# Performance work log

Hardware: AMD Instinct MI355X
Metric: run time of the kernel (lower is better)

The kernel has to match this reference:

```python
import jax, jax.numpy as jnp
import numpy as np

N_NODES = 50000
N_EDGES = 800000
IN_DIM = 128
EMB = 64
EDGE_DIM = 6
N_LAYERS = 4
OUT_DIM = 1


def setup_inputs() -> dict:
    key = jax.random.key(0)
    ks = jax.random.split(key, 20)
    s = 0.05
    inp = {
        "x": jax.random.normal(ks[0], (N_NODES, IN_DIM), jnp.float32),
        "edge_index": jax.random.randint(ks[1], (2, N_EDGES), 0, N_NODES, jnp.int64),
        "edge_attr": jax.random.normal(ks[2], (N_EDGES, EDGE_DIM), jnp.float32),
        # input projection
        "lin_in_w": jax.random.normal(ks[3], (IN_DIM, EMB), jnp.float32) * s,
        "lin_in_b": jnp.zeros((EMB,), jnp.float32),
        # stacked per-layer MLP params: message MLP psi: (2*EMB+EDGE_DIM)->EMB->EMB
        "msg_w1": jax.random.normal(ks[4], (N_LAYERS, 2 * EMB + EDGE_DIM, EMB), jnp.float32) * s,
        "msg_b1": jnp.zeros((N_LAYERS, EMB), jnp.float32),
        "msg_w2": jax.random.normal(ks[5], (N_LAYERS, EMB, EMB), jnp.float32) * s,
        "msg_b2": jnp.zeros((N_LAYERS, EMB), jnp.float32),
        # update MLP phi: (2*EMB)->EMB->EMB
        "upd_w1": jax.random.normal(ks[6], (N_LAYERS, 2 * EMB, EMB), jnp.float32) * s,
        "upd_b1": jnp.zeros((N_LAYERS, EMB), jnp.float32),
        "upd_w2": jax.random.normal(ks[7], (N_LAYERS, EMB, EMB), jnp.float32) * s,
        "upd_b2": jnp.zeros((N_LAYERS, EMB), jnp.float32),
        # output head
        "pred_w": jax.random.normal(ks[8], (EMB, OUT_DIM), jnp.float32) * s,
        "pred_b": jnp.zeros((OUT_DIM,), jnp.float32),
    }
    return inp


def reference(x, edge_index, edge_attr, lin_in_w, lin_in_b,
              msg_w1, msg_b1, msg_w2, msg_b2,
              upd_w1, upd_b1, upd_w2, upd_b2,
              pred_w, pred_b):
    n = x.shape[0]
    src = edge_index[0]  # h_j: source nodes
    dst = edge_index[1]  # h_i: target nodes (aggregation index in PyG default flow)
    h = x @ lin_in_w + lin_in_b  # (n, EMB)
    n_layers = msg_w1.shape[0]
    for l in range(n_layers):
        # message: psi([h_i, h_j, e_ij])  -> (E, EMB)
        m = jnp.concatenate([h[dst], h[src], edge_attr], axis=-1)
        m = jax.nn.relu(m @ msg_w1[l] + msg_b1[l])
        m = jax.nn.relu(m @ msg_w2[l] + msg_b2[l])
        # aggregate: scatter-add over target nodes
        agg = jax.ops.segment_sum(m, dst, num_segments=n)
        # update: phi([h, m_i]) with residual connection (h = h + conv(h))
        u = jnp.concatenate([h, agg], axis=-1)
        u = jax.nn.relu(u @ upd_w1[l] + upd_b1[l])
        u = jax.nn.relu(u @ upd_w2[l] + upd_b2[l])
        h = h + u
    out = h @ pred_w + pred_b  # (n, OUT_DIM)
    return jnp.sum(out, axis=-2)  # (OUT_DIM,)
```

## Files before the change

kernel.cpp:

```cpp
#include <hip/hip_runtime.h>


typedef __attribute__((ext_vector_type(8))) short short8;
typedef __attribute__((ext_vector_type(4))) float float4v;

__device__ __forceinline__ unsigned short f2bf(float f) {
    unsigned int u = __float_as_uint(f);
    unsigned int r = u + 0x7fff + ((u >> 16) & 1);
    return (unsigned short)(r >> 16);
}
__device__ __forceinline__ float bf2f(unsigned short u) {
    return __uint_as_float(((unsigned int)u) << 16);
}

#define MFMA16(a, b, c) __builtin_amdgcn_mfma_f32_16x16x32_bf16(a, b, c, 0, 0, 0)

struct bfpair { short hi, lo; };
__device__ __forceinline__ bfpair wsplit(float wv) {
    bfpair p;
    unsigned short h = f2bf(wv);
    float hf = __uint_as_float(((unsigned int)h) << 16);
    p.hi = (short)h;
    p.lo = (short)f2bf(wv - hf);
    return p;
}

#define WP_TOTAL 106496
#define OFF_IN   0
#define OFF_PRE(l)  (8192  + (l) * 8192)
#define OFF_MW2(l)  (40960 + (l) * 4096)
#define OFF_UW1(l)  (57344 + (l) * 8192)
#define OFF_UW2(l)  (90112 + (l) * 4096)

__global__ __launch_bounds__(256) void k_wprep(const float* __restrict__ lin_w,
        const float* __restrict__ mw1, const float* __restrict__ mw2,
        const float* __restrict__ uw1, const float* __restrict__ uw2,
        unsigned short* __restrict__ H, unsigned short* __restrict__ L) {
    const int tid = blockIdx.x * 256 + threadIdx.x;
    if (tid >= WP_TOTAL) return;
    float val;
    if (tid < 8192) {
        int rem = tid;
        int nt = rem >> 11, kf = (rem >> 9) & 3;
        int lane = (rem >> 3) & 63, j = rem & 7;
        int k = kf * 32 + (lane >> 4) * 8 + j;
        val = lin_w[k * 64 + nt * 16 + (lane & 15)];
    } else if (tid < 40960) {
        int t = tid - 8192, layer = t >> 13, rem = t & 8191;
        int nt = rem >> 10, kf = (rem >> 9) & 1;
        int lane = (rem >> 3) & 63, j = rem & 7;
        int k = kf * 32 + (lane >> 4) * 8 + j;
        const float* w1 = mw1 + (size_t)layer * 134 * 64;
        val = (nt < 4) ? w1[k * 64 + nt * 16 + (lane & 15)]
                       : w1[(64 + k) * 64 + (nt - 4) * 16 + (lane & 15)];
    } else if (tid < 57344) {
        int t = tid - 40960, layer = t >> 12, rem = t & 4095;
        int nt = rem >> 10, kf = (rem >> 9) & 1;
        int lane = (rem >> 3) & 63, j = rem & 7;
        int k = kf * 32 + (lane >> 4) * 8 + j;
        val = mw2[(size_t)layer * 4096 + k * 64 + nt * 16 + (lane & 15)];
    } else if (tid < 90112) {
        int t = tid - 57344, layer = t >> 13, rem = t & 8191;
        int nt = rem >> 11, kf = (rem >> 9) & 3;
        int lane = (rem >> 3) & 63, j = rem & 7;
        int k = kf * 32 + (lane >> 4) * 8 + j;
        val = uw1[(size_t)layer * 8192 + k * 64 + nt * 16 + (lane & 15)];
    } else {
        int t = tid - 90112, layer = t >> 12, rem = t & 4095;
        int nt = rem >> 10, kf = (rem >> 9) & 1;
        int lane = (rem >> 3) & 63, j = rem & 7;
        int k = kf * 32 + (lane >> 4) * 8 + j;
        val = uw2[(size_t)layer * 4096 + k * 64 + nt * 16 + (lane & 15)];
    }
    bfpair p = wsplit(val);
    H[tid] = (unsigned short)p.hi;
    L[tid] = (unsigned short)p.lo;
}

#define LOADFRAG(dst, arr, nt, KF, kf) \
    dst = *(const short8*)&arr[((((nt) * (KF)) + (kf)) * 64 + lane) * 8]

__global__ __launch_bounds__(256) void k_hist(const int* __restrict__ dst,
        int* __restrict__ deg, int nEdges) {
    int e = blockIdx.x * blockDim.x + threadIdx.x;
    if (e < nEdges) atomicAdd(&deg[dst[e]], 1);
}

__global__ __launch_bounds__(256) void k_scan1(const int* __restrict__ deg,
        int* __restrict__ local, int* __restrict__ bsum, int nNodes) {
    __shared__ int sm[256];
    const int t = threadIdx.x;
    const int n = blockIdx.x * 256 + t;
    int v = (n < nNodes) ? deg[n] : 0;
    sm[t] = v;
    __syncthreads();
    for (int off = 1; off < 256; off <<= 1) {
        int u = (t >= off) ? sm[t - off] : 0;
        __syncthreads();
        sm[t] += u;
        __syncthreads();
    }
    if (n < nNodes) local[n] = sm[t] - v;
    if (t == 255) bsum[blockIdx.x] = sm[255];
}

__global__ __launch_bounds__(256) void k_scan2(int* __restrict__ bsum, int nB) {
    __shared__ int sm[256];
    const int t = threadIdx.x;
    int v = (t < nB) ? bsum[t] : 0;
    sm[t] = v;
    __syncthreads();
    for (int off = 1; off < 256; off <<= 1) {
        int u = (t >= off) ? sm[t - off] : 0;
        __syncthreads();
        sm[t] += u;
        __syncthreads();
    }
    if (t < nB) bsum[t] = sm[t] - v;
}

__global__ __launch_bounds__(256) void k_scan3(const int* __restrict__ local,
        const int* __restrict__ bsum, int* __restrict__ cursor, int nNodes) {
    int n = blockIdx.x * 256 + threadIdx.x;
    if (n < nNodes) cursor[n] = bsum[blockIdx.x] + local[n];
}

__global__ __launch_bounds__(256) void k_scatter(const int* __restrict__ src,
        const int* __restrict__ dst, const float* __restrict__ ea,
        int* __restrict__ cursor, int* __restrict__ col_src,
        int* __restrict__ dst_s, float* __restrict__ ea_s, int nEdges) {
    int e = blockIdx.x * blockDim.x + threadIdx.x;
    if (e < nEdges) {
        int d = dst[e];
        int pos = atomicAdd(&cursor[d], 1);
        col_src[pos] = src[e];
        dst_s[pos] = d;
        const float* p = ea + (size_t)e * 6;
        float* q = ea_s + (size_t)pos * 6;
#pragma unroll
        for (int j = 0; j < 6; ++j) q[j] = p[j];
    }
}


__global__ __launch_bounds__(256) void k_in(const float* __restrict__ x,
        const unsigned short* __restrict__ wh, const unsigned short* __restrict__ wl,
        const float* __restrict__ bia, float* __restrict__ h, int nNodes) {
    const int lane = threadIdx.x & 63;
    const int wib  = threadIdx.x >> 6;
    const int quad = lane >> 4, col = lane & 15;
    __shared__ unsigned short sm[4][16 * 136];
    unsigned short* __restrict__ mt = sm[wib];

    short8 bh[4][4], bl[4][4];
#pragma unroll
    for (int nt = 0; nt < 4; ++nt)
#pragma unroll
        for (int kf = 0; kf < 4; ++kf) {
            LOADFRAG(bh[nt][kf], wh, nt, 4, kf);
            LOADFRAG(bl[nt][kf], wl, nt, 4, kf);
        }
    float bv[4];
#pragma unroll
    for (int nt = 0; nt < 4; ++nt) bv[nt] = bia[nt * 16 + col];

    const int nTiles = (nNodes + 15) >> 4;
    const int wid = blockIdx.x * 4 + wib;
    const int nw  = gridDim.x * 4;
    for (int tile = wid; tile < nTiles; tile += nw) {
        const int base = tile * 16;
#pragma unroll
        for (int j = 0; j < 16; ++j) {
            int row = min(base + j, nNodes - 1);
            mt[j * 136 + lane]      = f2bf(x[(size_t)row * 128 + lane]);
            mt[j * 136 + 64 + lane] = f2bf(x[(size_t)row * 128 + 64 + lane]);
        }
        __builtin_amdgcn_s_waitcnt(0);
        short8 a[4];
#pragma unroll
        for (int kf = 0; kf < 4; ++kf)
            a[kf] = *(const short8*)&mt[col * 136 + kf * 32 + quad * 8];
#pragma unroll
        for (int nt = 0; nt < 4; ++nt) {
            float4v c = {0.f, 0.f, 0.f, 0.f};
#pragma unroll
            for (int kf = 0; kf < 4; ++kf) c = MFMA16(a[kf], bh[nt][kf], c);
#pragma unroll
            for (int kf = 0; kf < 4; ++kf) c = MFMA16(a[kf], bl[nt][kf], c);
#pragma unroll
            for (int r = 0; r < 4; ++r) {
                int row = base + quad * 4 + r;
                if (row < nNodes)
                    h[(size_t)row * 64 + nt * 16 + col] = c[r] + bv[nt];
            }
        }
    }
}

__global__ __launch_bounds__(256) void k_pre(const float* __restrict__ h,
        const unsigned short* __restrict__ wh, const unsigned short* __restrict__ wl,
        const float* __restrict__ b1m,
        unsigned short* __restrict__ P, unsigned short* __restrict__ Q,
        int nNodes) {
    const int lane = threadIdx.x & 63;
    const int wib  = threadIdx.x >> 6;
    const int quad = lane >> 4, col = lane & 15;
    __shared__ unsigned short sm[4][16 * 72];
    unsigned short* __restrict__ mt = sm[wib];

    short8 bh[8][2], bl[8][2];
#pragma unroll
    for (int nt = 0; nt < 8; ++nt)
#pragma unroll
        for (int kf = 0; kf < 2; ++kf) {
            LOADFRAG(bh[nt][kf], wh, nt, 2, kf);
            LOADFRAG(bl[nt][kf], wl, nt, 2, kf);
        }
    float bv1[4];
#pragma unroll
    for (int nt = 0; nt < 4; ++nt) bv1[nt] = b1m[nt * 16 + col];

    const int nTiles = (nNodes + 15) >> 4;
    const int wid = blockIdx.x * 4 + wib;
    const int nw  = gridDim.x * 4;
    for (int tile = wid; tile < nTiles; tile += nw) {
        const int base = tile * 16;
#pragma unroll
        for (int j = 0; j < 16; ++j) {
            int row = min(base + j, nNodes - 1);
            mt[j * 72 + lane] = f2bf(h[(size_t)row * 64 + lane]);
        }
        __builtin_amdgcn_s_waitcnt(0);
        short8 a0 = *(const short8*)&mt[col * 72 + quad * 8];
        short8 a1 = *(const short8*)&mt[col * 72 + 32 + quad * 8];
#pragma unroll
        for (int nt = 0; nt < 8; ++nt) {
            float4v c = {0.f, 0.f, 0.f, 0.f};
            c = MFMA16(a0, bh[nt][0], c);
            c = MFMA16(a1, bh[nt][1], c);
            c = MFMA16(a0, bl[nt][0], c);
            c = MFMA16(a1, bl[nt][1], c);
            unsigned short* __restrict__ outp = (nt < 4) ? P : Q;
            const int nc = (nt & 3) * 16 + col;
            const float badd = (nt < 4) ? bv1[nt & 3] : 0.f;
#pragma unroll
            for (int r = 0; r < 4; ++r) {
                int row = base + quad * 4 + r;
                if (row < nNodes) outp[(size_t)row * 64 + nc] = f2bf(c[r] + badd);
            }
        }
    }
}

__global__ __launch_bounds__(256) void k_upd1(const float* __restrict__ h,
        const float* __restrict__ agg,
        const unsigned short* __restrict__ wh, const unsigned short* __restrict__ wl,
        const float* __restrict__ b1, float* __restrict__ tv, int nNodes) {
    const int lane = threadIdx.x & 63;
    const int wib  = threadIdx.x >> 6;
    const int quad = lane >> 4, col = lane & 15;
    __shared__ unsigned short sm[4][16 * 136];
    unsigned short* __restrict__ mt = sm[wib];

    short8 bh[4][4], bl[4][4];
#pragma unroll
    for (int nt = 0; nt < 4; ++nt)
#pragma unroll
        for (int kf = 0; kf < 4; ++kf) {
            LOADFRAG(bh[nt][kf], wh, nt, 4, kf);
            LOADFRAG(bl[nt][kf], wl, nt, 4, kf);
        }
    float bv[4];
#pragma unroll
    for (int nt = 0; nt < 4; ++nt) bv[nt] = b1[nt * 16 + col];

    const int nTiles = (nNodes + 15) >> 4;
    const int wid = blockIdx.x * 4 + wib;
    const int nw  = gridDim.x * 4;
    for (int tile = wid; tile < nTiles; tile += nw) {
        const int base = tile * 16;
#pragma unroll
        for (int j = 0; j < 16; ++j) {
            int row = min(base + j, nNodes - 1);
            mt[j * 136 + lane]      = f2bf(h[(size_t)row * 64 + lane]);
            mt[j * 136 + 64 + lane] = f2bf(agg[(size_t)row * 64 + lane]);
        }
        __builtin_amdgcn_s_waitcnt(0);
        short8 a[4];
#pragma unroll
        for (int kf = 0; kf < 4; ++kf)
            a[kf] = *(const short8*)&mt[col * 136 + kf * 32 + quad * 8];
#pragma unroll
        for (int nt = 0; nt < 4; ++nt) {
            float4v c = {0.f, 0.f, 0.f, 0.f};
#pragma unroll
            for (int kf = 0; kf < 4; ++kf) c = MFMA16(a[kf], bh[nt][kf], c);
#pragma unroll
            for (int kf = 0; kf < 4; ++kf) c = MFMA16(a[kf], bl[nt][kf], c);
#pragma unroll
            for (int r = 0; r < 4; ++r) {
                int row = base + quad * 4 + r;
                if (row < nNodes)
                    tv[(size_t)row * 64 + nt * 16 + col] = fmaxf(c[r] + bv[nt], 0.f);
            }
        }
    }
}

__global__ __launch_bounds__(256) void k_upd2(float* __restrict__ h,
        float* __restrict__ tv,
        const unsigned short* __restrict__ wh, const unsigned short* __restrict__ wl,
        const float* __restrict__ b2, float* __restrict__ colsum,
        int nNodes, int doCS) {
    const int lane = threadIdx.x & 63;
    const int wib  = threadIdx.x >> 6;
    const int quad = lane >> 4, col = lane & 15;
    __shared__ unsigned short sm[4][16 * 72];
    unsigned short* __restrict__ mt = sm[wib];

    short8 bh[4][2], bl[4][2];
#pragma unroll
    for (int nt = 0; nt < 4; ++nt)
#pragma unroll
        for (int kf = 0; kf < 2; ++kf) {
            LOADFRAG(bh[nt][kf], wh, nt, 2, kf);
            LOADFRAG(bl[nt][kf], wl, nt, 2, kf);
        }
    float bv[4];
#pragma unroll
    for (int nt = 0; nt < 4; ++nt) bv[nt] = b2[nt * 16 + col];

    float cs0 = 0.f, cs1 = 0.f, cs2 = 0.f, cs3 = 0.f;
    const int nTiles = (nNodes + 15) >> 4;
    const int wid = blockIdx.x * 4 + wib;
    const int nw  = gridDim.x * 4;
    for (int tile = wid; tile < nTiles; tile += nw) {
        const int base = tile * 16;
#pragma unroll
        for (int j = 0; j < 16; ++j) {
            int row = min(base + j, nNodes - 1);
            mt[j * 72 + lane] = f2bf(tv[(size_t)row * 64 + lane]);
        }
        __builtin_amdgcn_s_waitcnt(0);
#pragma unroll
        for (int j = 0; j < 16; ++j) {
            int row = base + j;
            if (row < nNodes) tv[(size_t)row * 64 + lane] = 0.f;
        }
        short8 a0 = *(const short8*)&mt[col * 72 + quad * 8];
        short8 a1 = *(const short8*)&mt[col * 72 + 32 + quad * 8];
#pragma unroll
        for (int nt = 0; nt < 4; ++nt) {
            float4v c = {0.f, 0.f, 0.f, 0.f};
            c = MFMA16(a0, bh[nt][0], c);
            c = MFMA16(a1, bh[nt][1], c);
            c = MFMA16(a0, bl[nt][0], c);
            c = MFMA16(a1, bl[nt][1], c);
#pragma unroll
            for (int r = 0; r < 4; ++r) {
                int row = base + quad * 4 + r;
                if (row < nNodes) {
                    float* hp = &h[(size_t)row * 64 + nt * 16 + col];
                    float hn = *hp + fmaxf(c[r] + bv[nt], 0.f);
                    *hp = hn;
                    cs0 += (nt == 0) ? hn : 0.f;
                    cs1 += (nt == 1) ? hn : 0.f;
                    cs2 += (nt == 2) ? hn : 0.f;
                    cs3 += (nt == 3) ? hn : 0.f;
                }
            }
        }
    }
    if (doCS) {
        cs0 += __shfl_xor(cs0, 16); cs0 += __shfl_xor(cs0, 32);
        cs1 += __shfl_xor(cs1, 16); cs1 += __shfl_xor(cs1, 32);
        cs2 += __shfl_xor(cs2, 16); cs2 += __shfl_xor(cs2, 32);
        cs3 += __shfl_xor(cs3, 16); cs3 += __shfl_xor(cs3, 32);
        const float tot = (quad == 0) ? cs0 : (quad == 1) ? cs1
                        : (quad == 2) ? cs2 : cs3;
        atomicAdd(&colsum[lane], tot);
    }
}

#define EST 72

__global__ __launch_bounds__(512, 6) void k_edge(const unsigned short* __restrict__ P,
        const unsigned short* __restrict__ Q, const float* __restrict__ ea_s,
        const int* __restrict__ col_src, const int* __restrict__ dst_s,
        const float* __restrict__ w1e,
        const unsigned short* __restrict__ wh, const unsigned short* __restrict__ wl,
        const float* __restrict__ b2,
        float* __restrict__ agg, int nEdges) {
    const int lane = threadIdx.x & 63;
    const int wib  = threadIdx.x >> 6;
    const int wid  = blockIdx.x * 8 + wib;
    const int nw   = gridDim.x * 8;
    const int quad = lane >> 4;
    const int col  = lane & 15;
    const int li   = lane & 31;

    __shared__ unsigned short m1b[8][32 * EST];
    __shared__ unsigned short wB[8192];
    unsigned short* __restrict__ mt = m1b[wib];

    {
        const short8* __restrict__ sH = (const short8*)wh;
        const short8* __restrict__ sL = (const short8*)wl;
        short8* __restrict__ dB = (short8*)wB;
        dB[threadIdx.x]       = sH[threadIdx.x];
        dB[512 + threadIdx.x] = sL[threadIdx.x];
    }
    __syncthreads();

    float w1ec[6];
#pragma unroll
    for (int j = 0; j < 6; ++j) w1ec[j] = w1e[j * 64 + lane];

    float b2v[4];
#pragma unroll
    for (int nt = 0; nt < 4; ++nt) b2v[nt] = b2[nt * 16 + col];

    const int nBatch = (nEdges + 31) >> 5;
    const int per = nBatch / nw, rem = nBatch % nw;
    const int btLo = wid * per + min(wid, rem);
    const int btHi = btLo + per + (wid < rem ? 1 : 0);

    for (int bt = btLo; bt < btHi; ++bt) {
        const int base = __builtin_amdgcn_readfirstlane(bt << 5);
        const int gidx = min(base + li, nEdges - 1);
        const int vdj = dst_s[gidx];
        const int vsj = col_src[gidx];
        const int vprev = __shfl_up(vdj, 1);
        unsigned long long bmask =
            __ballot(lane < 32 && (li == 0 || vdj != vprev));
        bmask |= (1ull << 32) | 1ull;

#pragma unroll
        for (int j = 0; j < 32; ++j) {
            const int d = __builtin_amdgcn_readlane(vdj, j);
            const int s = __builtin_amdgcn_readlane(vsj, j);
            const int idx = min(base + j, nEdges - 1);
            float t = bf2f(P[(size_t)d * 64 + lane]) +
                      bf2f(Q[(size_t)s * 64 + lane]);
            const float* eap = ea_s + (size_t)idx * 6;
#pragma unroll
            for (int jj = 0; jj < 6; ++jj) t = fmaf(eap[jj], w1ec[jj], t);
            mt[j * EST + lane] = f2bf(fmaxf(t, 0.f));
        }
        __builtin_amdgcn_s_waitcnt(0);

        short8 a00 = *(const short8*)&mt[col * EST + quad * 8];
        short8 a01 = *(const short8*)&mt[col * EST + 32 + quad * 8];
        short8 a10 = *(const short8*)&mt[(16 + col) * EST + quad * 8];
        short8 a11 = *(const short8*)&mt[(16 + col) * EST + 32 + quad * 8];

        float4v m2v[2][4];
#pragma unroll
        for (int nt = 0; nt < 4; ++nt) {
            const short8 h0 = *(const short8*)&wB[((nt * 2 + 0) * 64 + lane) * 8];
            const short8 h1 = *(const short8*)&wB[((nt * 2 + 1) * 64 + lane) * 8];
            const short8 l0 = *(const short8*)&wB[4096 + ((nt * 2 + 0) * 64 + lane) * 8];
            const short8 l1 = *(const short8*)&wB[4096 + ((nt * 2 + 1) * 64 + lane) * 8];
            float4v c0 = {0.f, 0.f, 0.f, 0.f};
            float4v c1 = {0.f, 0.f, 0.f, 0.f};
            c0 = MFMA16(a00, h0, c0);
            c0 = MFMA16(a01, h1, c0);
            c0 = MFMA16(a00, l0, c0);
            c0 = MFMA16(a01, l1, c0);
            c1 = MFMA16(a10, h0, c1);
            c1 = MFMA16(a11, h1, c1);
            c1 = MFMA16(a10, l0, c1);
            c1 = MFMA16(a11, l1, c1);
#pragma unroll
            for (int r = 0; r < 4; ++r) {
                const bool v0 = base + (quad * 4 + r) < nEdges;
                const bool v1 = base + 16 + (quad * 4 + r) < nEdges;
                m2v[0][nt][r] = v0 ? fmaxf(c0[r] + b2v[nt], 0.f) : 0.f;
                m2v[1][nt][r] = v1 ? fmaxf(c1[r] + b2v[nt], 0.f) : 0.f;
            }
        }

        int r0 = 0;
        while (r0 < 32) {
            const int nid = __builtin_amdgcn_readlane(vdj, r0);
            const int r1 = r0 + 1 + (int)__builtin_ctzll(bmask >> (r0 + 1));
            float s0 = 0.f, s1 = 0.f, s2 = 0.f, s3 = 0.f;
#pragma unroll
            for (int t = 0; t < 2; ++t)
#pragma unroll
                for (int r = 0; r < 4; ++r) {
                    const int R = t * 16 + quad * 4 + r;
                    const bool in = (R >= r0) && (R < r1);
                    s0 += in ? m2v[t][0][r] : 0.f;
                    s1 += in ? m2v[t][1][r] : 0.f;
                    s2 += in ? m2v[t][2][r] : 0.f;
                    s3 += in ? m2v[t][3][r] : 0.f;
                }
            s0 += __shfl_xor(s0, 16); s0 += __shfl_xor(s0, 32);
            s1 += __shfl_xor(s1, 16); s1 += __shfl_xor(s1, 32);
            s2 += __shfl_xor(s2, 16); s2 += __shfl_xor(s2, 32);
            s3 += __shfl_xor(s3, 16); s3 += __shfl_xor(s3, 32);
            const float tot = (quad == 0) ? s0 : (quad == 1) ? s1
                            : (quad == 2) ? s2 : s3;
            atomicAdd(&agg[(size_t)nid * 64 + lane], tot);
            r0 = r1;
        }
    }
}

__global__ void k_out(const float* __restrict__ colsum, const float* __restrict__ pw,
                      const float* __restrict__ pb, float* __restrict__ out, int nNodes) {
    const int lane = threadIdx.x;
    float v = colsum[lane] * pw[lane];
#pragma unroll
    for (int off = 32; off; off >>= 1) v += __shfl_down(v, off);
    if (lane == 0) out[0] = v + (float)nNodes * pb[0];
}

extern "C" void kernel_launch(void* const* d_in, const int* in_sizes, int n_in,
                              void* d_out, int out_size, void* d_ws, size_t ws_size,
                              hipStream_t stream) {
    const float* x     = (const float*)d_in[0];
    const int*   ei    = (const int*)d_in[1];
    const float* ea    = (const float*)d_in[2];
    const float* lin_w = (const float*)d_in[3];
    const float* lin_b = (const float*)d_in[4];
    const float* mw1   = (const float*)d_in[5];
    const float* mb1   = (const float*)d_in[6];
    const float* mw2   = (const float*)d_in[7];
    const float* mb2   = (const float*)d_in[8];
    const float* uw1   = (const float*)d_in[9];
    const float* ub1   = (const float*)d_in[10];
    const float* uw2   = (const float*)d_in[11];
    const float* ub2   = (const float*)d_in[12];
    const float* pw    = (const float*)d_in[13];
    const float* pb    = (const float*)d_in[14];

    const int nNodes = in_sizes[0] / 128;
    const int nEdges = in_sizes[1] / 2;
    const int* src = ei;
    const int* dst = ei + nEdges;

    float* h       = (float*)d_ws;
    float* agg     = h   + (size_t)nNodes * 64;
    float* ea_s    = agg + (size_t)nNodes * 64;
    float* colsum  = ea_s + (size_t)nEdges * 6;
    unsigned short* Pb  = (unsigned short*)(colsum + 64);
    unsigned short* Qb  = Pb + (size_t)nNodes * 64;
    unsigned short* wpH = Qb + (size_t)nNodes * 64;
    unsigned short* wpL = wpH + WP_TOTAL;
    int*   deg     = (int*)(wpL + WP_TOTAL);
    int*   cursor  = deg + nNodes;
    int*   local   = cursor + nNodes;
    int*   bsum    = local + nNodes;
    int*   col_src = bsum + 256;
    int*   dst_s   = col_src + nEdges;

    const int NB_T    = 392;
    const int NB_EDGE = 768;
    const int NB_FLAT = (nEdges + 255) / 256;
    const int NB_SCAN = (nNodes + 255) / 256;

    hipMemsetAsync(deg, 0, (size_t)nNodes * sizeof(int), stream);
    hipMemsetAsync(colsum, 0, 64 * sizeof(float), stream);
    hipMemsetAsync(agg, 0, (size_t)nNodes * 64 * sizeof(float), stream);
    k_hist<<<NB_FLAT, 256, 0, stream>>>(dst, deg, nEdges);
    k_scan1<<<NB_SCAN, 256, 0, stream>>>(deg, local, bsum, nNodes);
    k_scan2<<<1, 256, 0, stream>>>(bsum, NB_SCAN);
    k_scan3<<<NB_SCAN, 256, 0, stream>>>(local, bsum, cursor, nNodes);
    k_scatter<<<NB_FLAT, 256, 0, stream>>>(src, dst, ea, cursor, col_src, dst_s, ea_s, nEdges);
    k_wprep<<<(WP_TOTAL + 255) / 256, 256, 0, stream>>>(lin_w, mw1, mw2, uw1, uw2, wpH, wpL);

    k_in<<<NB_T, 256, 0, stream>>>(x, wpH + OFF_IN, wpL + OFF_IN, lin_b, h, nNodes);

    for (int l = 0; l < 4; ++l) {
        k_pre<<<NB_T, 256, 0, stream>>>(h, wpH + OFF_PRE(l), wpL + OFF_PRE(l),
            mb1 + l * 64, Pb, Qb, nNodes);
        k_edge<<<NB_EDGE, 512, 0, stream>>>(Pb, Qb, ea_s, col_src, dst_s,
            mw1 + (size_t)l * 134 * 64 + 128 * 64,
            wpH + OFF_MW2(l), wpL + OFF_MW2(l), mb2 + l * 64, agg, nEdges);
        k_upd1<<<NB_T, 256, 0, stream>>>(h, agg,
            wpH + OFF_UW1(l), wpL + OFF_UW1(l), ub1 + l * 64, agg, nNodes);
        k_upd2<<<NB_T, 256, 0, stream>>>(h, agg,
            wpH + OFF_UW2(l), wpL + OFF_UW2(l), ub2 + l * 64,
            colsum, nNodes, (l == 3) ? 1 : 0);
    }

    k_out<<<1, 64, 0, stream>>>(colsum, pw, pb, (float*)d_out, nNodes);
}
```

Measured before the change: 639.2 us.

## Bucket CSR edges by source half to improve gather locality

```diff
diff --git a/kernel.cpp b/kernel.cpp
--- a/kernel.cpp
+++ b/kernel.cpp
@@ -80,18 +80,22 @@
 #define LOADFRAG(dst, arr, nt, KF, kf) \
     dst = *(const short8*)&arr[((((nt) * (KF)) + (kf)) * 64 + lane) * 8]
 
-__global__ __launch_bounds__(256) void k_hist(const int* __restrict__ dst,
-        int* __restrict__ deg, int nEdges) {
+__global__ __launch_bounds__(256) void k_hist(const int* __restrict__ src,
+        const int* __restrict__ dst, int* __restrict__ deg,
+        int nEdges, int nNodes, int split) {
     int e = blockIdx.x * blockDim.x + threadIdx.x;
-    if (e < nEdges) atomicAdd(&deg[dst[e]], 1);
+    if (e < nEdges) {
+        int bin = dst[e] + (src[e] >= split ? nNodes : 0);
+        atomicAdd(&deg[bin], 1);
+    }
 }
 
 __global__ __launch_bounds__(256) void k_scan1(const int* __restrict__ deg,
-        int* __restrict__ local, int* __restrict__ bsum, int nNodes) {
+        int* __restrict__ local, int* __restrict__ bsum, int nBins) {
     __shared__ int sm[256];
     const int t = threadIdx.x;
     const int n = blockIdx.x * 256 + t;
-    int v = (n < nNodes) ? deg[n] : 0;
+    int v = (n < nBins) ? deg[n] : 0;
     sm[t] = v;
     __syncthreads();
     for (int off = 1; off < 256; off <<= 1) {
@@ -100,15 +104,22 @@
         sm[t] += u;
         __syncthreads();
     }
-    if (n < nNodes) local[n] = sm[t] - v;
+    if (n < nBins) local[n] = sm[t] - v;
     if (t == 255) bsum[blockIdx.x] = sm[255];
 }
 
 __global__ __launch_bounds__(256) void k_scan2(int* __restrict__ bsum, int nB) {
     __shared__ int sm[256];
     const int t = threadIdx.x;
-    int v = (t < nB) ? bsum[t] : 0;
-    sm[t] = v;
+    int vals[8];
+    int s = 0;
+#pragma unroll
+    for (int k = 0; k < 8; ++k) {
+        int i = t * 8 + k;
+        vals[k] = (i < nB) ? bsum[i] : 0;
+        s += vals[k];
+    }
+    sm[t] = s;
     __syncthreads();
     for (int off = 1; off < 256; off <<= 1) {
         int u = (t >= off) ? sm[t - off] : 0;
@@ -116,24 +127,34 @@
         sm[t] += u;
         __syncthreads();
     }
-    if (t < nB) bsum[t] = sm[t] - v;
+    int run = sm[t] - s;
+#pragma unroll
+    for (int k = 0; k < 8; ++k) {
+        int i = t * 8 + k;
+        int old = vals[k];
+        if (i < nB) bsum[i] = run;
+        run += old;
+    }
 }
 
 __global__ __launch_bounds__(256) void k_scan3(const int* __restrict__ local,
-        const int* __restrict__ bsum, int* __restrict__ cursor, int nNodes) {
+        const int* __restrict__ bsum, int* __restrict__ cursor, int nBins) {
     int n = blockIdx.x * 256 + threadIdx.x;
-    if (n < nNodes) cursor[n] = bsum[blockIdx.x] + local[n];
+    if (n < nBins) cursor[n] = bsum[blockIdx.x] + local[n];
 }
 
 __global__ __launch_bounds__(256) void k_scatter(const int* __restrict__ src,
         const int* __restrict__ dst, const float* __restrict__ ea,
         int* __restrict__ cursor, int* __restrict__ col_src,
-        int* __restrict__ dst_s, float* __restrict__ ea_s, int nEdges) {
+        int* __restrict__ dst_s, float* __restrict__ ea_s,
+        int nEdges, int nNodes, int split) {
     int e = blockIdx.x * blockDim.x + threadIdx.x;
     if (e < nEdges) {
         int d = dst[e];
-        int pos = atomicAdd(&cursor[d], 1);
-        col_src[pos] = src[e];
+        int s = src[e];
+        int bin = d + (s >= split ? nNodes : 0);
+        int pos = atomicAdd(&cursor[bin], 1);
+        col_src[pos] = s;
         dst_s[pos] = d;
         const float* p = ea + (size_t)e * 6;
         float* q = ea_s + (size_t)pos * 6;
@@ -540,6 +561,8 @@
     const int nEdges = in_sizes[1] / 2;
     const int* src = ei;
     const int* dst = ei + nEdges;
+    const int nBins = 2 * nNodes;
+    const int split = nNodes / 2;
 
     float* h       = (float*)d_ws;
     float* agg     = h   + (size_t)nNodes * 64;
@@ -550,25 +573,26 @@
     unsigned short* wpH = Qb + (size_t)nNodes * 64;
     unsigned short* wpL = wpH + WP_TOTAL;
     int*   deg     = (int*)(wpL + WP_TOTAL);
-    int*   cursor  = deg + nNodes;
-    int*   local   = cursor + nNodes;
-    int*   bsum    = local + nNodes;
-    int*   col_src = bsum + 256;
+    int*   cursor  = deg + nBins;
+    int*   local   = cursor + nBins;
+    int*   bsum    = local + nBins;
+    int*   col_src = bsum + 2048;
     int*   dst_s   = col_src + nEdges;
 
     const int NB_T    = 392;
     const int NB_EDGE = 768;
     const int NB_FLAT = (nEdges + 255) / 256;
-    const int NB_SCAN = (nNodes + 255) / 256;
-
-    hipMemsetAsync(deg, 0, (size_t)nNodes * sizeof(int), stream);
+    const int NB_SCAN = (nBins + 255) / 256;
+
+    hipMemsetAsync(deg, 0, (size_t)nBins * sizeof(int), stream);
     hipMemsetAsync(colsum, 0, 64 * sizeof(float), stream);
     hipMemsetAsync(agg, 0, (size_t)nNodes * 64 * sizeof(float), stream);
-    k_hist<<<NB_FLAT, 256, 0, stream>>>(dst, deg, nEdges);
-    k_scan1<<<NB_SCAN, 256, 0, stream>>>(deg, local, bsum, nNodes);
+    k_hist<<<NB_FLAT, 256, 0, stream>>>(src, dst, deg, nEdges, nNodes, split);
+    k_scan1<<<NB_SCAN, 256, 0, stream>>>(deg, local, bsum, nBins);
     k_scan2<<<1, 256, 0, stream>>>(bsum, NB_SCAN);
-    k_scan3<<<NB_SCAN, 256, 0, stream>>>(local, bsum, cursor, nNodes);
-    k_scatter<<<NB_FLAT, 256, 0, stream>>>(src, dst, ea, cursor, col_src, dst_s, ea_s, nEdges);
+    k_scan3<<<NB_SCAN, 256, 0, stream>>>(local, bsum, cursor, nBins);
+    k_scatter<<<NB_FLAT, 256, 0, stream>>>(src, dst, ea, cursor, col_src, dst_s, ea_s,
+                                           nEdges, nNodes, split);
     k_wprep<<<(WP_TOTAL + 255) / 256, 256, 0, stream>>>(lin_w, mw1, mw2, uw1, uw2, wpH, wpL);
 
     k_in<<<NB_T, 256, 0, stream>>>(x, wpH + OFF_IN, wpL + OFF_IN, lin_b, h, nNodes);
```

After: 657.6 us. 1.03x slower.
